# Kernel optimization log

Measured on AMD Instinct MI355X. Metric: run time of the kernel, lower is better.

## Reference

```python
import jax, jax.numpy as jnp
import numpy as np

CLIP_MIN = 0.0
CLIP_MAX = 1.0
B, T, F, E, CD = 64, 48, 128, 64, 32


def setup_inputs() -> dict:
    key = jax.random.key(0)
    ks = jax.random.split(key, 8)
    return {
        "input_x": jax.random.uniform(ks[0], (B, T, F), dtype=jnp.float32),
        "mask": jax.random.randint(ks[1], (B, T, F), 0, 2, dtype=jnp.int32),
        "embed0": jax.random.normal(ks[2], (F, E), dtype=jnp.float32) * 0.1,
        "embed1": jax.random.normal(ks[3], (F, E), dtype=jnp.float32) * 0.1,
        "embed_missing": jax.random.normal(ks[4], (F, E), dtype=jnp.float32) * 0.1,
        "attention_f_w": jax.random.normal(ks[5], (F, E), dtype=jnp.float32) * 0.1,
        "attention_f_b": jnp.zeros((F,), dtype=jnp.float32),
        "compress_w": jax.random.normal(ks[6], (2 * E, CD), dtype=jnp.float32) * 0.1,
    }


def reference(input_x, mask, embed0, embed1, embed_missing, attention_f_w, attention_f_b, compress_w):
    b, t, f = input_x.shape
    # new_mask: feature observed anywhere in time -> [b, 1, f, 1] (broadcasts over time)
    m = (jnp.sum(mask, axis=-2) != 0).astype(input_x.dtype)[:, None, :, None]
    x = input_x[..., None]  # [b, t, f, 1]
    # interval embedding c: [b, t, f, e]
    c0 = (x - m * CLIP_MIN) * embed0
    c1 = (m * CLIP_MAX - x) * embed1
    c = (c0 + c1) / (CLIP_MAX - CLIP_MIN) + (1.0 - m) * embed_missing
    # pairwise scores: sum_e c_i * c_j * w_i + b_i  (avoids [b,t,f,f,e] materialization)
    scores = jnp.einsum("btie,btje->btij", c * attention_f_w, c) + attention_f_b[:, None]
    scores = jnp.clip(scores, -5.0, 5.0)
    off_diag = 1.0 - jnp.eye(f, dtype=c.dtype)
    masked_exps = jnp.exp(scores) * off_diag
    attn = masked_exps / (jnp.sum(masked_exps, axis=-1, keepdims=True) + 1e-8)  # [b,t,f,f]
    # weighted aggregation: sum_j attn_ij * (c_i * c_j) = c_i * (attn @ c)_i
    agg = c * jnp.einsum("btij,btje->btie", attn, c)
    a = jax.nn.relu(jnp.concatenate([c, agg], axis=-1))  # [b,t,f,2e]
    out = jnp.einsum("btfk,kd->btfd", a, compress_w)
    return out.reshape(b, t, f * compress_w.shape[-1])
```

## Files before the change

### kernel.cpp

```cpp
#include <hip/hip_runtime.h>

#define NB 64
#define NT 48
#define NF 128
#define NE 64
#define NCD 32

#define LOG2E 1.4426950408889634f
#define SCLO -7.213475204444817f
#define SCHI  7.213475204444817f

typedef __attribute__((ext_vector_type(8))) short bf16x8;
typedef __attribute__((ext_vector_type(4))) float f32x4;
typedef __attribute__((ext_vector_type(2))) uint u32x2;

#define WS_MFLAG 0
#define WS_DB    32768
#define WS_E1B   49152
#define WS_EMB   65536
#define WS_WLB   81920
#define WS_WT    98304
#define WS_BL    106496

__device__ __forceinline__ ushort f2bf(float x) {
    union { float f; uint u; } v; v.f = x;
    uint r = v.u + 0x7fffu + ((v.u >> 16) & 1u);
    return (ushort)(r >> 16);
}
__device__ __forceinline__ uint pk_bf16(float lo, float hi) {
    uint r; asm("v_cvt_pk_bf16_f32 %0, %1, %2" : "=v"(r) : "v"(lo), "v"(hi)); return r;
}
__device__ __forceinline__ float bflo(uint u) { union { uint u; float f; } v; v.u = u << 16; return v.f; }
__device__ __forceinline__ float bfhi(uint u) { union { uint u; float f; } v; v.u = u & 0xffff0000u; return v.f; }

#define TRR(dst, addr, IMM) \
    asm volatile("ds_read_b64_tr_b16 %0, %1 offset:" IMM : "=v"(dst) : "v"(addr))

__global__ __launch_bounds__(256) void prep_kernel(
    const int* __restrict__ mask, const float* __restrict__ e0, const float* __restrict__ e1,
    const float* __restrict__ em, const float* __restrict__ aw, const float* __restrict__ ab,
    const float* __restrict__ cw,
    uint* __restrict__ mflag, ushort* __restrict__ db, ushort* __restrict__ e1b,
    ushort* __restrict__ emb, ushort* __restrict__ wlb, ushort* __restrict__ wt,
    float* __restrict__ bl)
{
    const int blk = blockIdx.x, tid = threadIdx.x;
    if (blk < 32) {
        int idx = blk * 256 + tid;
        float e1v = e1[idx];
        e1b[idx] = f2bf(e1v);
        emb[idx] = f2bf(em[idx]);
        db[idx]  = f2bf(e0[idx] - e1v);
        wlb[idx] = f2bf(aw[idx] * LOG2E);
    } else if (blk < 64) {
        int idx = (blk - 32) * 256 + tid;
        int b = idx >> 7, f = idx & 127;
        const int* p = mask + b * (NT * NF) + f;
        int s = 0;
#pragma unroll
        for (int t = 0; t < NT; ++t) s += p[t * NF];
        mflag[idx] = (s != 0) ? 1u : 0u;
    } else if (blk < 80) {
        int idx = (blk - 64) * 256 + tid;
        int k = idx >> 5, d = idx & 31;
        wt[d * 128 + k] = f2bf(cw[idx]);
    } else {
        if (tid < NF) bl[tid] = ab[tid] * LOG2E;
    }
}

__global__ __launch_bounds__(512, 4) void fused_kernel(
    const float* __restrict__ input_x, const uint* __restrict__ mflag,
    const ushort* __restrict__ db, const ushort* __restrict__ e1b, const ushort* __restrict__ emb,
    const ushort* __restrict__ wlb, const float* __restrict__ blog,
    const ushort* __restrict__ wt, float* __restrict__ out)
{
    __shared__ ushort sC[2 * 9248];
    __shared__ ushort sPA[2 * 8 * 1152];

    const int tid = threadIdx.x;
    const int blk = blockIdx.x;
    const int b   = blk / 24;
    const int bt0 = b * NT + (blk % 24) * 2;
    const int bt1 = bt0 + 1;

    const int wv = tid >> 6, ln = tid & 63;
    const int lr = ln & 15, lg = ln >> 4;
    const int i0 = wv << 4, irow = i0 + lr;

    const float bl = blog[irow];
    const float x0 = input_x[bt0 * NF + irow];
    const float x1 = input_x[bt1 * NF + irow];
    const ushort* Mrow = (mflag[b * NF + irow] ? e1b : emb) + irow * NE;
    const ushort* Drow = db + irow * NE;
    const ushort* Wrow = wlb + irow * NE;

    const int sbase = (lg >> 1) * 2312 + (lr >> 2) * 72 + (lr & 3) * 16 + (lg & 1) * 8;

    ushort* sC0 = sC;
    ushort* sC1 = sC + 9248;
    ushort* strip0 = &sPA[wv * 1152];
    ushort* strip1 = &sPA[9216 + wv * 1152];

    bf16x8 cwf0[2], cwf1[2];
#pragma unroll
    for (int ks = 0; ks < 2; ++ks) {
        const int eo = ks * 32 + lg * 8;
        uint d4[4], m4[4], w4[4];
        *(uint4*)d4 = *(const uint4*)(Drow + eo);
        *(uint4*)m4 = *(const uint4*)(Mrow + eo);
        *(uint4*)w4 = *(const uint4*)(Wrow + eo);
        uint cb0[4], cb1[4];
        union { uint u[4]; bf16x8 v; } cw0, cw1;
#pragma unroll
        for (int j = 0; j < 4; ++j) {
            float dlo = bflo(d4[j]), dhi = bfhi(d4[j]);
            float mlo = bflo(m4[j]), mhi = bfhi(m4[j]);
            float wlo = bflo(w4[j]), whi = bfhi(w4[j]);
            float c0lo = fmaf(x0, dlo, mlo), c0hi = fmaf(x0, dhi, mhi);
            float c1lo = fmaf(x1, dlo, mlo), c1hi = fmaf(x1, dhi, mhi);
            cb0[j] = pk_bf16(c0lo, c0hi);
            cb1[j] = pk_bf16(c1lo, c1hi);
            cw0.u[j] = pk_bf16(c0lo * wlo, c0hi * whi);
            cw1.u[j] = pk_bf16(c1lo * wlo, c1hi * whi);
        }
        cwf0[ks] = cw0.v; cwf1[ks] = cw1.v;
        *(uint4*)&sC0[sbase + wv * 288 + ks * 4624] = *(uint4*)cb0;
        *(uint4*)&sC1[sbase + wv * 288 + ks * 4624] = *(uint4*)cb1;
    }
    __syncthreads();

    auto run_S = [&](const ushort* base, bf16x8 w0, bf16x8 w1, f32x4* st) {
#pragma unroll
        for (int jt = 0; jt < 8; ++jt) {
            f32x4 a = (f32x4){bl, bl, bl, bl};
            bf16x8 a0 = *(bf16x8*)&base[sbase + jt * 288];
            a = __builtin_amdgcn_mfma_f32_16x16x32_bf16(a0, w0, a, 0, 0, 0);
            bf16x8 a1 = *(bf16x8*)&base[sbase + jt * 288 + 4624];
            a = __builtin_amdgcn_mfma_f32_16x16x32_bf16(a1, w1, a, 0, 0, 0);
            st[jt] = a;
        }
    };
    auto run_SM = [&](f32x4* st, uint* pp) -> float {
        float rs0 = 0.f, rs1 = 0.f, rs2 = 0.f, rs3 = 0.f;
#pragma unroll
        for (int jt = 0; jt < 8; ++jt) {
            f32x4 v = st[jt];
            float e0 = exp2f(__builtin_amdgcn_fmed3f(v[0], SCLO, SCHI));
            float e1 = exp2f(__builtin_amdgcn_fmed3f(v[1], SCLO, SCHI));
            float e2 = exp2f(__builtin_amdgcn_fmed3f(v[2], SCLO, SCHI));
            float e3 = exp2f(__builtin_amdgcn_fmed3f(v[3], SCLO, SCHI));
            if (jt == wv) {
                const bool on = (lg == (lr >> 2));
                e0 = (on && (lr & 3) == 0) ? 0.f : e0;
                e1 = (on && (lr & 3) == 1) ? 0.f : e1;
                e2 = (on && (lr & 3) == 2) ? 0.f : e2;
                e3 = (on && (lr & 3) == 3) ? 0.f : e3;
            }
            rs0 += e0; rs1 += e1; rs2 += e2; rs3 += e3;
            pp[2 * jt]     = pk_bf16(e0, e1);
            pp[2 * jt + 1] = pk_bf16(e2, e3);
        }
        float rs = (rs0 + rs1) + (rs2 + rs3);
        rs += __shfl_xor(rs, 16);
        rs += __shfl_xor(rs, 32);
        return 1.0f / (rs + 1e-8f);
    };
    auto run_AGG = [&](ushort* strip, const ushort* base, const uint* pp, f32x4* ag) {
#pragma unroll
        for (int et = 0; et < 4; ++et) ag[et] = (f32x4){0.f, 0.f, 0.f, 0.f};
        const uint baddr = (uint)(uintptr_t)base;
#pragma unroll
        for (int ks = 0; ks < 4; ++ks) {
#pragma unroll
            for (int h = 0; h < 2; ++h) {
                const int jt = ks * 2 + h;
                *(u32x2*)&strip[lr * 72 + h * 16 + lg * 4] = (u32x2){pp[2 * jt], pp[2 * jt + 1]};
            }
            bf16x8 pf = *(bf16x8*)&strip[lr * 72 + lg * 8];
            const uint tb = baddr + 2u * (uint)(144 * lg + lr) + 1152u * (uint)ks;
            u32x2 c0a, c0b, c1a, c1b, c2a, c2b, c3a, c3b;
            TRR(c0a, tb, "0");     TRR(c0b, tb, "144");
            TRR(c1a, tb, "4624");  TRR(c1b, tb, "4768");
            TRR(c2a, tb, "9248");  TRR(c2b, tb, "9392");
            TRR(c3a, tb, "13872"); TRR(c3b, tb, "14016");
            asm volatile("s_waitcnt lgkmcnt(0)" ::: "memory");
            __builtin_amdgcn_sched_barrier(0);
            union { u32x2 d[2]; bf16x8 v; } a0, a1, a2, a3;
            a0.d[0] = c0a; a0.d[1] = c0b;
            a1.d[0] = c1a; a1.d[1] = c1b;
            a2.d[0] = c2a; a2.d[1] = c2b;
            a3.d[0] = c3a; a3.d[1] = c3b;
            ag[0] = __builtin_amdgcn_mfma_f32_16x16x32_bf16(a0.v, pf, ag[0], 0, 0, 0);
            ag[1] = __builtin_amdgcn_mfma_f32_16x16x32_bf16(a1.v, pf, ag[1], 0, 0, 0);
            ag[2] = __builtin_amdgcn_mfma_f32_16x16x32_bf16(a2.v, pf, ag[2], 0, 0, 0);
            ag[3] = __builtin_amdgcn_mfma_f32_16x16x32_bf16(a3.v, pf, ag[3], 0, 0, 0);
        }
    };
    auto run_EPI = [&](ushort* strip, const ushort* base, f32x4* ag, float inv) {
        const int ebase = (wv * 4 + (lr >> 2)) * 72 + (lr & 3) * 16 + lg * 4;
#pragma unroll
        for (int et = 0; et < 4; ++et) {
            u32x2 cb2 = *(u32x2*)&base[ebase + et * 2312];
            float a0 = fmaxf(ag[et][0] * inv * bflo(cb2.x), 0.f);
            float a1 = fmaxf(ag[et][1] * inv * bfhi(cb2.x), 0.f);
            float a2 = fmaxf(ag[et][2] * inv * bflo(cb2.y), 0.f);
            float a3 = fmaxf(ag[et][3] * inv * bfhi(cb2.y), 0.f);
            *(u32x2*)&strip[lr * 72 + et * 16 + lg * 4] = (u32x2){pk_bf16(a0, a1), pk_bf16(a2, a3)};
        }
    };
    auto run_OUT = [&](const ushort* strip, const ushort* base, const bf16x8* wf, int bt) {
        f32x4 oc[2];
        oc[0] = (f32x4){0.f, 0.f, 0.f, 0.f};
        oc[1] = (f32x4){0.f, 0.f, 0.f, 0.f};
#pragma unroll
        for (int ks = 0; ks < 4; ++ks) {
            bf16x8 afr;
            if (ks < 2) {
                const uint4 cc = *(uint4*)&base[sbase + wv * 288 + ks * 4624];
                union { uint u[4]; bf16x8 v; } rl;
                asm("v_pk_max_i16 %0, %1, 0" : "=v"(rl.u[0]) : "v"(cc.x));
                asm("v_pk_max_i16 %0, %1, 0" : "=v"(rl.u[1]) : "v"(cc.y));
                asm("v_pk_max_i16 %0, %1, 0" : "=v"(rl.u[2]) : "v"(cc.z));
                asm("v_pk_max_i16 %0, %1, 0" : "=v"(rl.u[3]) : "v"(cc.w));
                afr = rl.v;
            } else {
                afr = *(bf16x8*)&strip[lr * 72 + (ks - 2) * 32 + lg * 8];
            }
            oc[0] = __builtin_amdgcn_mfma_f32_16x16x32_bf16(afr, wf[ks * 2 + 0], oc[0], 0, 0, 0);
            oc[1] = __builtin_amdgcn_mfma_f32_16x16x32_bf16(afr, wf[ks * 2 + 1], oc[1], 0, 0, 0);
        }
        float* op = out + bt * (NF * NCD);
#pragma unroll
        for (int dt = 0; dt < 2; ++dt)
#pragma unroll
            for (int r = 0; r < 4; ++r)
                op[(i0 + lg * 4 + r) * NCD + dt * 16 + lr] = oc[dt][r];
    };

    f32x4 st0[8], st1[8];
    uint pp0[16], pp1[16];
    f32x4 ag0[4], ag1[4];

    run_S(sC0, cwf0[0], cwf0[1], st0);
    const float inv0 = run_SM(st0, pp0);
    run_S(sC1, cwf1[0], cwf1[1], st1);
    const float inv1 = run_SM(st1, pp1);

    run_AGG(strip0, sC0, pp0, ag0);
    run_EPI(strip0, sC0, ag0, inv0);
    run_AGG(strip1, sC1, pp1, ag1);

    bf16x8 wf[8];
#pragma unroll
    for (int ks = 0; ks < 4; ++ks)
#pragma unroll
        for (int dt = 0; dt < 2; ++dt)
            wf[ks * 2 + dt] = *(const bf16x8*)(wt + (dt * 16 + lr) * 128 + ks * 32 + lg * 8);

    run_EPI(strip1, sC1, ag1, inv1);
    run_OUT(strip0, sC0, wf, bt0);
    run_OUT(strip1, sC1, wf, bt1);
}

extern "C" void kernel_launch(void* const* d_in, const int* in_sizes, int n_in,
                              void* d_out, int out_size, void* d_ws, size_t ws_size,
                              hipStream_t stream) {
    const float* input_x       = (const float*)d_in[0];
    const int*   mask          = (const int*)d_in[1];
    const float* embed0        = (const float*)d_in[2];
    const float* embed1        = (const float*)d_in[3];
    const float* embed_missing = (const float*)d_in[4];
    const float* attn_w        = (const float*)d_in[5];
    const float* attn_b        = (const float*)d_in[6];
    const float* compress_w    = (const float*)d_in[7];
    float* out = (float*)d_out;

    char* ws = (char*)d_ws;
    uint*   mflag = (uint*)(ws + WS_MFLAG);
    ushort* dbp   = (ushort*)(ws + WS_DB);
    ushort* e1bp  = (ushort*)(ws + WS_E1B);
    ushort* embp  = (ushort*)(ws + WS_EMB);
    ushort* wlbp  = (ushort*)(ws + WS_WLB);
    ushort* wtp   = (ushort*)(ws + WS_WT);
    float*  blp   = (float*)(ws + WS_BL);

    hipLaunchKernelGGL(prep_kernel, dim3(81), dim3(256), 0, stream,
                       mask, embed0, embed1, embed_missing, attn_w, attn_b, compress_w,
                       mflag, dbp, e1bp, embp, wlbp, wtp, blp);
    hipLaunchKernelGGL(fused_kernel, dim3(NB * NT / 2), dim3(512), 0, stream,
                       input_x, mflag, dbp, e1bp, embp, wlbp, blp, wtp, out);
}
```

Measured before the change: 44.14 us.

## Software-pipeline softmax, aggregation and epilogue across the two timesteps

Replaces the sequential per-timestep lambdas with interleaved code. Tile 0's softmax exp work is placed between tile 1's score MFMAs, and tile 1's softmax is placed between tile 0's aggregation MFMAs. Tile 0's epilogue likewise overlaps tile 1's aggregation, and the two output GEMMs are interleaved. The aim is to hide VALU/transcendental and LDS latency behind MFMA work, at the cost of higher register pressure and a dependence on the compiler keeping the intended order.

```diff
diff --git a/kernel.cpp b/kernel.cpp
--- a/kernel.cpp
+++ b/kernel.cpp
@@ -35,6 +35,24 @@
 
 #define TRR(dst, addr, IMM) \
     asm volatile("ds_read_b64_tr_b16 %0, %1 offset:" IMM : "=v"(dst) : "v"(addr))
+
+#define SM_STEP(ST, PP, JT, RSA) do {                                     \
+    f32x4 v_ = ST[JT];                                                    \
+    float e0_ = exp2f(__builtin_amdgcn_fmed3f(v_[0], SCLO, SCHI));        \
+    float e1_ = exp2f(__builtin_amdgcn_fmed3f(v_[1], SCLO, SCHI));        \
+    float e2_ = exp2f(__builtin_amdgcn_fmed3f(v_[2], SCLO, SCHI));        \
+    float e3_ = exp2f(__builtin_amdgcn_fmed3f(v_[3], SCLO, SCHI));        \
+    if ((JT) == wv) {                                                     \
+        const bool on_ = (lg == (lr >> 2));                               \
+        e0_ = (on_ && (lr & 3) == 0) ? 0.f : e0_;                         \
+        e1_ = (on_ && (lr & 3) == 1) ? 0.f : e1_;                         \
+        e2_ = (on_ && (lr & 3) == 2) ? 0.f : e2_;                         \
+        e3_ = (on_ && (lr & 3) == 3) ? 0.f : e3_;                         \
+    }                                                                     \
+    RSA[0] += e0_; RSA[1] += e1_; RSA[2] += e2_; RSA[3] += e3_;           \
+    PP[2 * (JT)]     = pk_bf16(e0_, e1_);                                 \
+    PP[2 * (JT) + 1] = pk_bf16(e2_, e3_);                                 \
+} while (0)
 
 __global__ __launch_bounds__(256) void prep_kernel(
     const int* __restrict__ mask, const float* __restrict__ e0, const float* __restrict__ e1,
@@ -130,126 +148,69 @@
     }
     __syncthreads();
 
-    auto run_S = [&](const ushort* base, bf16x8 w0, bf16x8 w1, f32x4* st) {
-#pragma unroll
-        for (int jt = 0; jt < 8; ++jt) {
-            f32x4 a = (f32x4){bl, bl, bl, bl};
-            bf16x8 a0 = *(bf16x8*)&base[sbase + jt * 288];
-            a = __builtin_amdgcn_mfma_f32_16x16x32_bf16(a0, w0, a, 0, 0, 0);
-            bf16x8 a1 = *(bf16x8*)&base[sbase + jt * 288 + 4624];
-            a = __builtin_amdgcn_mfma_f32_16x16x32_bf16(a1, w1, a, 0, 0, 0);
-            st[jt] = a;
-        }
-    };
-    auto run_SM = [&](f32x4* st, uint* pp) -> float {
-        float rs0 = 0.f, rs1 = 0.f, rs2 = 0.f, rs3 = 0.f;
-#pragma unroll
-        for (int jt = 0; jt < 8; ++jt) {
-            f32x4 v = st[jt];
-            float e0 = exp2f(__builtin_amdgcn_fmed3f(v[0], SCLO, SCHI));
-            float e1 = exp2f(__builtin_amdgcn_fmed3f(v[1], SCLO, SCHI));
-            float e2 = exp2f(__builtin_amdgcn_fmed3f(v[2], SCLO, SCHI));
-            float e3 = exp2f(__builtin_amdgcn_fmed3f(v[3], SCLO, SCHI));
-            if (jt == wv) {
-                const bool on = (lg == (lr >> 2));
-                e0 = (on && (lr & 3) == 0) ? 0.f : e0;
-                e1 = (on && (lr & 3) == 1) ? 0.f : e1;
-                e2 = (on && (lr & 3) == 2) ? 0.f : e2;
-                e3 = (on && (lr & 3) == 3) ? 0.f : e3;
-            }
-            rs0 += e0; rs1 += e1; rs2 += e2; rs3 += e3;
-            pp[2 * jt]     = pk_bf16(e0, e1);
-            pp[2 * jt + 1] = pk_bf16(e2, e3);
-        }
-        float rs = (rs0 + rs1) + (rs2 + rs3);
-        rs += __shfl_xor(rs, 16);
-        rs += __shfl_xor(rs, 32);
-        return 1.0f / (rs + 1e-8f);
-    };
-    auto run_AGG = [&](ushort* strip, const ushort* base, const uint* pp, f32x4* ag) {
-#pragma unroll
-        for (int et = 0; et < 4; ++et) ag[et] = (f32x4){0.f, 0.f, 0.f, 0.f};
-        const uint baddr = (uint)(uintptr_t)base;
-#pragma unroll
-        for (int ks = 0; ks < 4; ++ks) {
-#pragma unroll
-            for (int h = 0; h < 2; ++h) {
-                const int jt = ks * 2 + h;
-                *(u32x2*)&strip[lr * 72 + h * 16 + lg * 4] = (u32x2){pp[2 * jt], pp[2 * jt + 1]};
-            }
-            bf16x8 pf = *(bf16x8*)&strip[lr * 72 + lg * 8];
-            const uint tb = baddr + 2u * (uint)(144 * lg + lr) + 1152u * (uint)ks;
-            u32x2 c0a, c0b, c1a, c1b, c2a, c2b, c3a, c3b;
-            TRR(c0a, tb, "0");     TRR(c0b, tb, "144");
-            TRR(c1a, tb, "4624");  TRR(c1b, tb, "4768");
-            TRR(c2a, tb, "9248");  TRR(c2b, tb, "9392");
-            TRR(c3a, tb, "13872"); TRR(c3b, tb, "14016");
-            asm volatile("s_waitcnt lgkmcnt(0)" ::: "memory");
-            __builtin_amdgcn_sched_barrier(0);
-            union { u32x2 d[2]; bf16x8 v; } a0, a1, a2, a3;
-            a0.d[0] = c0a; a0.d[1] = c0b;
-            a1.d[0] = c1a; a1.d[1] = c1b;
-            a2.d[0] = c2a; a2.d[1] = c2b;
-            a3.d[0] = c3a; a3.d[1] = c3b;
-            ag[0] = __builtin_amdgcn_mfma_f32_16x16x32_bf16(a0.v, pf, ag[0], 0, 0, 0);
-            ag[1] = __builtin_amdgcn_mfma_f32_16x16x32_bf16(a1.v, pf, ag[1], 0, 0, 0);
-            ag[2] = __builtin_amdgcn_mfma_f32_16x16x32_bf16(a2.v, pf, ag[2], 0, 0, 0);
-            ag[3] = __builtin_amdgcn_mfma_f32_16x16x32_bf16(a3.v, pf, ag[3], 0, 0, 0);
-        }
-    };
-    auto run_EPI = [&](ushort* strip, const ushort* base, f32x4* ag, float inv) {
-        const int ebase = (wv * 4 + (lr >> 2)) * 72 + (lr & 3) * 16 + lg * 4;
-#pragma unroll
-        for (int et = 0; et < 4; ++et) {
-            u32x2 cb2 = *(u32x2*)&base[ebase + et * 2312];
-            float a0 = fmaxf(ag[et][0] * inv * bflo(cb2.x), 0.f);
-            float a1 = fmaxf(ag[et][1] * inv * bfhi(cb2.x), 0.f);
-            float a2 = fmaxf(ag[et][2] * inv * bflo(cb2.y), 0.f);
-            float a3 = fmaxf(ag[et][3] * inv * bfhi(cb2.y), 0.f);
-            *(u32x2*)&strip[lr * 72 + et * 16 + lg * 4] = (u32x2){pk_bf16(a0, a1), pk_bf16(a2, a3)};
-        }
-    };
-    auto run_OUT = [&](const ushort* strip, const ushort* base, const bf16x8* wf, int bt) {
-        f32x4 oc[2];
-        oc[0] = (f32x4){0.f, 0.f, 0.f, 0.f};
-        oc[1] = (f32x4){0.f, 0.f, 0.f, 0.f};
-#pragma unroll
-        for (int ks = 0; ks < 4; ++ks) {
-            bf16x8 afr;
-            if (ks < 2) {
-                const uint4 cc = *(uint4*)&base[sbase + wv * 288 + ks * 4624];
-                union { uint u[4]; bf16x8 v; } rl;
-                asm("v_pk_max_i16 %0, %1, 0" : "=v"(rl.u[0]) : "v"(cc.x));
-                asm("v_pk_max_i16 %0, %1, 0" : "=v"(rl.u[1]) : "v"(cc.y));
-                asm("v_pk_max_i16 %0, %1, 0" : "=v"(rl.u[2]) : "v"(cc.z));
-                asm("v_pk_max_i16 %0, %1, 0" : "=v"(rl.u[3]) : "v"(cc.w));
-                afr = rl.v;
-            } else {
-                afr = *(bf16x8*)&strip[lr * 72 + (ks - 2) * 32 + lg * 8];
-            }
-            oc[0] = __builtin_amdgcn_mfma_f32_16x16x32_bf16(afr, wf[ks * 2 + 0], oc[0], 0, 0, 0);
-            oc[1] = __builtin_amdgcn_mfma_f32_16x16x32_bf16(afr, wf[ks * 2 + 1], oc[1], 0, 0, 0);
-        }
-        float* op = out + bt * (NF * NCD);
-#pragma unroll
-        for (int dt = 0; dt < 2; ++dt)
-#pragma unroll
-            for (int r = 0; r < 4; ++r)
-                op[(i0 + lg * 4 + r) * NCD + dt * 16 + lr] = oc[dt][r];
-    };
-
     f32x4 st0[8], st1[8];
     uint pp0[16], pp1[16];
+    float rsa0[4] = {0.f, 0.f, 0.f, 0.f}, rsa1[4] = {0.f, 0.f, 0.f, 0.f};
+
+#pragma unroll
+    for (int jt = 0; jt < 8; ++jt) {
+        f32x4 a = (f32x4){bl, bl, bl, bl};
+        bf16x8 a0 = *(bf16x8*)&sC0[sbase + jt * 288];
+        a = __builtin_amdgcn_mfma_f32_16x16x32_bf16(a0, cwf0[0], a, 0, 0, 0);
+        bf16x8 a1 = *(bf16x8*)&sC0[sbase + jt * 288 + 4624];
+        a = __builtin_amdgcn_mfma_f32_16x16x32_bf16(a1, cwf0[1], a, 0, 0, 0);
+        st0[jt] = a;
+    }
+
+#pragma unroll
+    for (int jt = 0; jt < 8; ++jt) {
+        f32x4 a = (f32x4){bl, bl, bl, bl};
+        bf16x8 a0 = *(bf16x8*)&sC1[sbase + jt * 288];
+        a = __builtin_amdgcn_mfma_f32_16x16x32_bf16(a0, cwf1[0], a, 0, 0, 0);
+        bf16x8 a1 = *(bf16x8*)&sC1[sbase + jt * 288 + 4624];
+        a = __builtin_amdgcn_mfma_f32_16x16x32_bf16(a1, cwf1[1], a, 0, 0, 0);
+        st1[jt] = a;
+        SM_STEP(st0, pp0, jt, rsa0);
+    }
+    float rs0 = (rsa0[0] + rsa0[1]) + (rsa0[2] + rsa0[3]);
+    rs0 += __shfl_xor(rs0, 16);
+    rs0 += __shfl_xor(rs0, 32);
+    const float inv0 = 1.0f / (rs0 + 1e-8f);
+
+    const uint b0addr = (uint)(uintptr_t)sC0;
+    const uint b1addr = (uint)(uintptr_t)sC1;
     f32x4 ag0[4], ag1[4];
-
-    run_S(sC0, cwf0[0], cwf0[1], st0);
-    const float inv0 = run_SM(st0, pp0);
-    run_S(sC1, cwf1[0], cwf1[1], st1);
-    const float inv1 = run_SM(st1, pp1);
-
-    run_AGG(strip0, sC0, pp0, ag0);
-    run_EPI(strip0, sC0, ag0, inv0);
-    run_AGG(strip1, sC1, pp1, ag1);
+#pragma unroll
+    for (int et = 0; et < 4; ++et) { ag0[et] = (f32x4){0.f, 0.f, 0.f, 0.f}; ag1[et] = (f32x4){0.f, 0.f, 0.f, 0.f}; }
+#pragma unroll
+    for (int ks = 0; ks < 4; ++ks) {
+        *(u32x2*)&strip0[lr * 72 + lg * 4]      = (u32x2){pp0[4 * ks],     pp0[4 * ks + 1]};
+        *(u32x2*)&strip0[lr * 72 + 16 + lg * 4] = (u32x2){pp0[4 * ks + 2], pp0[4 * ks + 3]};
+        bf16x8 pf = *(bf16x8*)&strip0[lr * 72 + lg * 8];
+        const uint tb = b0addr + 2u * (uint)(144 * lg + lr) + 1152u * (uint)ks;
+        u32x2 c0a, c0b, c1a, c1b, c2a, c2b, c3a, c3b;
+        TRR(c0a, tb, "0");     TRR(c0b, tb, "144");
+        TRR(c1a, tb, "4624");  TRR(c1b, tb, "4768");
+        TRR(c2a, tb, "9248");  TRR(c2b, tb, "9392");
+        TRR(c3a, tb, "13872"); TRR(c3b, tb, "14016");
+        SM_STEP(st1, pp1, 2 * ks, rsa1);
+        SM_STEP(st1, pp1, 2 * ks + 1, rsa1);
+        asm volatile("s_waitcnt lgkmcnt(0)" ::: "memory");
+        __builtin_amdgcn_sched_barrier(0);
+        union { u32x2 d[2]; bf16x8 v; } a0, a1, a2, a3;
+        a0.d[0] = c0a; a0.d[1] = c0b;
+        a1.d[0] = c1a; a1.d[1] = c1b;
+        a2.d[0] = c2a; a2.d[1] = c2b;
+        a3.d[0] = c3a; a3.d[1] = c3b;
+        ag0[0] = __builtin_amdgcn_mfma_f32_16x16x32_bf16(a0.v, pf, ag0[0], 0, 0, 0);
+        ag0[1] = __builtin_amdgcn_mfma_f32_16x16x32_bf16(a1.v, pf, ag0[1], 0, 0, 0);
+        ag0[2] = __builtin_amdgcn_mfma_f32_16x16x32_bf16(a2.v, pf, ag0[2], 0, 0, 0);
+        ag0[3] = __builtin_amdgcn_mfma_f32_16x16x32_bf16(a3.v, pf, ag0[3], 0, 0, 0);
+    }
+    float rs1 = (rsa1[0] + rsa1[1]) + (rsa1[2] + rsa1[3]);
+    rs1 += __shfl_xor(rs1, 16);
+    rs1 += __shfl_xor(rs1, 32);
+    const float inv1 = 1.0f / (rs1 + 1e-8f);
 
     bf16x8 wf[8];
 #pragma unroll
@@ -258,9 +219,86 @@
         for (int dt = 0; dt < 2; ++dt)
             wf[ks * 2 + dt] = *(const bf16x8*)(wt + (dt * 16 + lr) * 128 + ks * 32 + lg * 8);
 
-    run_EPI(strip1, sC1, ag1, inv1);
-    run_OUT(strip0, sC0, wf, bt0);
-    run_OUT(strip1, sC1, wf, bt1);
+    const int ebase = (wv * 4 + (lr >> 2)) * 72 + (lr & 3) * 16 + lg * 4;
+#pragma unroll
+    for (int ks = 0; ks < 4; ++ks) {
+        *(u32x2*)&strip1[lr * 72 + lg * 4]      = (u32x2){pp1[4 * ks],     pp1[4 * ks + 1]};
+        *(u32x2*)&strip1[lr * 72 + 16 + lg * 4] = (u32x2){pp1[4 * ks + 2], pp1[4 * ks + 3]};
+        bf16x8 pf = *(bf16x8*)&strip1[lr * 72 + lg * 8];
+        const uint tb = b1addr + 2u * (uint)(144 * lg + lr) + 1152u * (uint)ks;
+        u32x2 c0a, c0b, c1a, c1b, c2a, c2b, c3a, c3b;
+        TRR(c0a, tb, "0");     TRR(c0b, tb, "144");
+        TRR(c1a, tb, "4624");  TRR(c1b, tb, "4768");
+        TRR(c2a, tb, "9248");  TRR(c2b, tb, "9392");
+        TRR(c3a, tb, "13872"); TRR(c3b, tb, "14016");
+        {
+            u32x2 cb2 = *(u32x2*)&sC0[ebase + ks * 2312];
+            float a0f = fmaxf(ag0[ks][0] * inv0 * bflo(cb2.x), 0.f);
+            float a1f = fmaxf(ag0[ks][1] * inv0 * bfhi(cb2.x), 0.f);
+            float a2f = fmaxf(ag0[ks][2] * inv0 * bflo(cb2.y), 0.f);
+            float a3f = fmaxf(ag0[ks][3] * inv0 * bfhi(cb2.y), 0.f);
+            *(u32x2*)&strip0[lr * 72 + ks * 16 + lg * 4] = (u32x2){pk_bf16(a0f, a1f), pk_bf16(a2f, a3f)};
+        }
+        asm volatile("s_waitcnt lgkmcnt(0)" ::: "memory");
+        __builtin_amdgcn_sched_barrier(0);
+        union { u32x2 d[2]; bf16x8 v; } a0, a1, a2, a3;
+        a0.d[0] = c0a; a0.d[1] = c0b;
+        a1.d[0] = c1a; a1.d[1] = c1b;
+        a2.d[0] = c2a; a2.d[1] = c2b;
+        a3.d[0] = c3a; a3.d[1] = c3b;
+        ag1[0] = __builtin_amdgcn_mfma_f32_16x16x32_bf16(a0.v, pf, ag1[0], 0, 0, 0);
+        ag1[1] = __builtin_amdgcn_mfma_f32_16x16x32_bf16(a1.v, pf, ag1[1], 0, 0, 0);
+        ag1[2] = __builtin_amdgcn_mfma_f32_16x16x32_bf16(a2.v, pf, ag1[2], 0, 0, 0);
+        ag1[3] = __builtin_amdgcn_mfma_f32_16x16x32_bf16(a3.v, pf, ag1[3], 0, 0, 0);
+    }
+
+#pragma unroll
+    for (int et = 0; et < 4; ++et) {
+        u32x2 cb2 = *(u32x2*)&sC1[ebase + et * 2312];
+        float a0f = fmaxf(ag1[et][0] * inv1 * bflo(cb2.x), 0.f);
+        float a1f = fmaxf(ag1[et][1] * inv1 * bfhi(cb2.x), 0.f);
+        float a2f = fmaxf(ag1[et][2] * inv1 * bflo(cb2.y), 0.f);
+        float a3f = fmaxf(ag1[et][3] * inv1 * bfhi(cb2.y), 0.f);
+        *(u32x2*)&strip1[lr * 72 + et * 16 + lg * 4] = (u32x2){pk_bf16(a0f, a1f), pk_bf16(a2f, a3f)};
+    }
+
+    f32x4 oc0[2], oc1[2];
+    oc0[0] = (f32x4){0.f, 0.f, 0.f, 0.f}; oc0[1] = (f32x4){0.f, 0.f, 0.f, 0.f};
+    oc1[0] = (f32x4){0.f, 0.f, 0.f, 0.f}; oc1[1] = (f32x4){0.f, 0.f, 0.f, 0.f};
+#pragma unroll
+    for (int ks = 0; ks < 4; ++ks) {
+        bf16x8 afr0, afr1;
+        if (ks < 2) {
+            const uint4 cc0 = *(uint4*)&sC0[sbase + wv * 288 + ks * 4624];
+            const uint4 cc1 = *(uint4*)&sC1[sbase + wv * 288 + ks * 4624];
+            union { uint u[4]; bf16x8 v; } r0, r1;
+            asm("v_pk_max_i16 %0, %1, 0" : "=v"(r0.u[0]) : "v"(cc0.x));
+            asm("v_pk_max_i16 %0, %1, 0" : "=v"(r0.u[1]) : "v"(cc0.y));
+            asm("v_pk_max_i16 %0, %1, 0" : "=v"(r0.u[2]) : "v"(cc0.z));
+            asm("v_pk_max_i16 %0, %1, 0" : "=v"(r0.u[3]) : "v"(cc0.w));
+            asm("v_pk_max_i16 %0, %1, 0" : "=v"(r1.u[0]) : "v"(cc1.x));
+            asm("v_pk_max_i16 %0, %1, 0" : "=v"(r1.u[1]) : "v"(cc1.y));
+            asm("v_pk_max_i16 %0, %1, 0" : "=v"(r1.u[2]) : "v"(cc1.z));
+            asm("v_pk_max_i16 %0, %1, 0" : "=v"(r1.u[3]) : "v"(cc1.w));
+            afr0 = r0.v; afr1 = r1.v;
+        } else {
+            afr0 = *(bf16x8*)&strip0[lr * 72 + (ks - 2) * 32 + lg * 8];
+            afr1 = *(bf16x8*)&strip1[lr * 72 + (ks - 2) * 32 + lg * 8];
+        }
+        oc0[0] = __builtin_amdgcn_mfma_f32_16x16x32_bf16(afr0, wf[ks * 2 + 0], oc0[0], 0, 0, 0);
+        oc0[1] = __builtin_amdgcn_mfma_f32_16x16x32_bf16(afr0, wf[ks * 2 + 1], oc0[1], 0, 0, 0);
+        oc1[0] = __builtin_amdgcn_mfma_f32_16x16x32_bf16(afr1, wf[ks * 2 + 0], oc1[0], 0, 0, 0);
+        oc1[1] = __builtin_amdgcn_mfma_f32_16x16x32_bf16(afr1, wf[ks * 2 + 1], oc1[1], 0, 0, 0);
+    }
+    float* op0 = out + bt0 * (NF * NCD);
+    float* op1 = out + bt1 * (NF * NCD);
+#pragma unroll
+    for (int dt = 0; dt < 2; ++dt)
+#pragma unroll
+        for (int r = 0; r < 4; ++r) {
+            op0[(i0 + lg * 4 + r) * NCD + dt * 16 + lr] = oc0[dt][r];
+            op1[(i0 + lg * 4 + r) * NCD + dt * 16 + lr] = oc1[dt][r];
+        }
 }
 
 extern "C" void kernel_launch(void* const* d_in, const int* in_sizes, int n_in,
```

Result: slower. 47.26 us (+7.1%).

## Replace LDS strip transposes with permlane32 swaps and permute compress weights

Applied to the files above, without the earlier changes.

Removes the per-wave shared-memory strip that converted MFMA accumulator layout into operand layout for the attention probabilities and for the aggregated features. It uses v_permlane32_swap register exchanges instead, and remaps the C-operand transpose-read addresses to match. The compress weight rows for the second half of K are permuted in the prep kernel to absorb the resulting element order. This cuts LDS writes and reads plus a sync dependency and frees LDS for occupancy, at the cost of a more intricate index mapping that must stay consistent across three places.

```diff
diff --git a/kernel.cpp b/kernel.cpp
--- a/kernel.cpp
+++ b/kernel.cpp
@@ -35,6 +35,8 @@
 
 #define TRR(dst, addr, IMM) \
     asm volatile("ds_read_b64_tr_b16 %0, %1 offset:" IMM : "=v"(dst) : "v"(addr))
+
+#define PLSWAP(a, b) asm("v_permlane32_swap_b32 %0, %1" : "+v"(a), "+v"(b))
 
 __global__ __launch_bounds__(256) void prep_kernel(
     const int* __restrict__ mask, const float* __restrict__ e0, const float* __restrict__ e1,
@@ -63,7 +65,13 @@
     } else if (blk < 80) {
         int idx = (blk - 64) * 256 + tid;
         int k = idx >> 5, d = idx & 31;
-        wt[d * 128 + k] = f2bf(cw[idx]);
+        int kd;
+        if (k < 64) kd = k;
+        else {
+            int kk = k - 64;
+            kd = 64 + ((kk & 51) | ((kk & 4) << 1) | ((kk & 8) >> 1));
+        }
+        wt[d * 128 + kd] = f2bf(cw[idx]);
     } else {
         if (tid < NF) bl[tid] = ab[tid] * LOG2E;
     }
@@ -76,7 +84,6 @@
     const ushort* __restrict__ wt, float* __restrict__ out)
 {
     __shared__ ushort sC[2 * 9248];
-    __shared__ ushort sPA[2 * 8 * 1152];
 
     const int tid = threadIdx.x;
     const int blk = blockIdx.x;
@@ -99,8 +106,6 @@
 
     ushort* sC0 = sC;
     ushort* sC1 = sC + 9248;
-    ushort* strip0 = &sPA[wv * 1152];
-    ushort* strip1 = &sPA[9216 + wv * 1152];
 
     bf16x8 cwf0[2], cwf1[2];
 #pragma unroll
@@ -166,19 +171,19 @@
         rs += __shfl_xor(rs, 32);
         return 1.0f / (rs + 1e-8f);
     };
-    auto run_AGG = [&](ushort* strip, const ushort* base, const uint* pp, f32x4* ag) {
+    auto run_AGG = [&](const ushort* base, uint* pp, f32x4* ag) {
 #pragma unroll
         for (int et = 0; et < 4; ++et) ag[et] = (f32x4){0.f, 0.f, 0.f, 0.f};
-        const uint baddr = (uint)(uintptr_t)base;
+        const uint tb0 = (uint)(uintptr_t)base
+                       + 2u * (uint)(72 * (((lg >> 1) << 2) + (lg & 1)) + lr);
 #pragma unroll
         for (int ks = 0; ks < 4; ++ks) {
-#pragma unroll
-            for (int h = 0; h < 2; ++h) {
-                const int jt = ks * 2 + h;
-                *(u32x2*)&strip[lr * 72 + h * 16 + lg * 4] = (u32x2){pp[2 * jt], pp[2 * jt + 1]};
-            }
-            bf16x8 pf = *(bf16x8*)&strip[lr * 72 + lg * 8];
-            const uint tb = baddr + 2u * (uint)(144 * lg + lr) + 1152u * (uint)ks;
+            uint X0 = pp[4 * ks], X1 = pp[4 * ks + 1], X2 = pp[4 * ks + 2], X3 = pp[4 * ks + 3];
+            PLSWAP(X0, X2);
+            PLSWAP(X1, X3);
+            union { uint u[4]; bf16x8 v; } pf;
+            pf.u[0] = X0; pf.u[1] = X1; pf.u[2] = X2; pf.u[3] = X3;
+            const uint tb = tb0 + 1152u * (uint)ks;
             u32x2 c0a, c0b, c1a, c1b, c2a, c2b, c3a, c3b;
             TRR(c0a, tb, "0");     TRR(c0b, tb, "144");
             TRR(c1a, tb, "4624");  TRR(c1b, tb, "4768");
@@ -191,25 +196,26 @@
             a1.d[0] = c1a; a1.d[1] = c1b;
             a2.d[0] = c2a; a2.d[1] = c2b;
             a3.d[0] = c3a; a3.d[1] = c3b;
-            ag[0] = __builtin_amdgcn_mfma_f32_16x16x32_bf16(a0.v, pf, ag[0], 0, 0, 0);
-            ag[1] = __builtin_amdgcn_mfma_f32_16x16x32_bf16(a1.v, pf, ag[1], 0, 0, 0);
-            ag[2] = __builtin_amdgcn_mfma_f32_16x16x32_bf16(a2.v, pf, ag[2], 0, 0, 0);
-            ag[3] = __builtin_amdgcn_mfma_f32_16x16x32_bf16(a3.v, pf, ag[3], 0, 0, 0);
-        }
-    };
-    auto run_EPI = [&](ushort* strip, const ushort* base, f32x4* ag, float inv) {
+            ag[0] = __builtin_amdgcn_mfma_f32_16x16x32_bf16(a0.v, pf.v, ag[0], 0, 0, 0);
+            ag[1] = __builtin_amdgcn_mfma_f32_16x16x32_bf16(a1.v, pf.v, ag[1], 0, 0, 0);
+            ag[2] = __builtin_amdgcn_mfma_f32_16x16x32_bf16(a2.v, pf.v, ag[2], 0, 0, 0);
+            ag[3] = __builtin_amdgcn_mfma_f32_16x16x32_bf16(a3.v, pf.v, ag[3], 0, 0, 0);
+        }
+    };
+    auto run_EPI = [&](const ushort* base, f32x4* ag, float inv, uint* aa) {
         const int ebase = (wv * 4 + (lr >> 2)) * 72 + (lr & 3) * 16 + lg * 4;
 #pragma unroll
         for (int et = 0; et < 4; ++et) {
             u32x2 cb2 = *(u32x2*)&base[ebase + et * 2312];
-            float a0 = fmaxf(ag[et][0] * inv * bflo(cb2.x), 0.f);
-            float a1 = fmaxf(ag[et][1] * inv * bfhi(cb2.x), 0.f);
-            float a2 = fmaxf(ag[et][2] * inv * bflo(cb2.y), 0.f);
-            float a3 = fmaxf(ag[et][3] * inv * bfhi(cb2.y), 0.f);
-            *(u32x2*)&strip[lr * 72 + et * 16 + lg * 4] = (u32x2){pk_bf16(a0, a1), pk_bf16(a2, a3)};
-        }
-    };
-    auto run_OUT = [&](const ushort* strip, const ushort* base, const bf16x8* wf, int bt) {
+            float a0f = fmaxf(ag[et][0] * inv * bflo(cb2.x), 0.f);
+            float a1f = fmaxf(ag[et][1] * inv * bfhi(cb2.x), 0.f);
+            float a2f = fmaxf(ag[et][2] * inv * bflo(cb2.y), 0.f);
+            float a3f = fmaxf(ag[et][3] * inv * bfhi(cb2.y), 0.f);
+            aa[2 * et]     = pk_bf16(a0f, a1f);
+            aa[2 * et + 1] = pk_bf16(a2f, a3f);
+        }
+    };
+    auto run_OUT = [&](const ushort* base, uint* aa, const bf16x8* wf, int bt) {
         f32x4 oc[2];
         oc[0] = (f32x4){0.f, 0.f, 0.f, 0.f};
         oc[1] = (f32x4){0.f, 0.f, 0.f, 0.f};
@@ -225,7 +231,13 @@
                 asm("v_pk_max_i16 %0, %1, 0" : "=v"(rl.u[3]) : "v"(cc.w));
                 afr = rl.v;
             } else {
-                afr = *(bf16x8*)&strip[lr * 72 + (ks - 2) * 32 + lg * 8];
+                const int kk = ks - 2;
+                uint Y0 = aa[4 * kk], Y1 = aa[4 * kk + 1], Y2 = aa[4 * kk + 2], Y3 = aa[4 * kk + 3];
+                PLSWAP(Y0, Y2);
+                PLSWAP(Y1, Y3);
+                union { uint u[4]; bf16x8 v; } af;
+                af.u[0] = Y0; af.u[1] = Y1; af.u[2] = Y2; af.u[3] = Y3;
+                afr = af.v;
             }
             oc[0] = __builtin_amdgcn_mfma_f32_16x16x32_bf16(afr, wf[ks * 2 + 0], oc[0], 0, 0, 0);
             oc[1] = __builtin_amdgcn_mfma_f32_16x16x32_bf16(afr, wf[ks * 2 + 1], oc[1], 0, 0, 0);
@@ -241,15 +253,16 @@
     f32x4 st0[8], st1[8];
     uint pp0[16], pp1[16];
     f32x4 ag0[4], ag1[4];
+    uint aa0[8], aa1[8];
 
     run_S(sC0, cwf0[0], cwf0[1], st0);
     const float inv0 = run_SM(st0, pp0);
     run_S(sC1, cwf1[0], cwf1[1], st1);
     const float inv1 = run_SM(st1, pp1);
 
-    run_AGG(strip0, sC0, pp0, ag0);
-    run_EPI(strip0, sC0, ag0, inv0);
-    run_AGG(strip1, sC1, pp1, ag1);
+    run_AGG(sC0, pp0, ag0);
+    run_EPI(sC0, ag0, inv0, aa0);
+    run_AGG(sC1, pp1, ag1);
 
     bf16x8 wf[8];
 #pragma unroll
@@ -258,9 +271,9 @@
         for (int dt = 0; dt < 2; ++dt)
             wf[ks * 2 + dt] = *(const bf16x8*)(wt + (dt * 16 + lr) * 128 + ks * 32 + lg * 8);
 
-    run_EPI(strip1, sC1, ag1, inv1);
-    run_OUT(strip0, sC0, wf, bt0);
-    run_OUT(strip1, sC1, wf, bt1);
+    run_EPI(sC1, ag1, inv1, aa1);
+    run_OUT(sC0, aa0, wf, bt0);
+    run_OUT(sC1, aa1, wf, bt1);
 }
 
 extern "C" void kernel_launch(void* const* d_in, const int* in_sizes, int n_in,
```

New measurement: 43.11 us. -2.3%, faster.
